# Kernel optimization log

Measured on AMD Instinct MI355X. Metric: run time of the kernel, lower is better.

Reference implementation:

```python
import jax, jax.numpy as jnp
import numpy as np

K = 32          # k_value
NUM_CLASSES = 10


def setup_inputs() -> dict:
    key = jax.random.key(0)
    k1, k2, k3 = jax.random.split(key, 3)
    queries = jax.random.normal(k1, (1024, 64), dtype=jnp.float32)
    train_data = jax.random.normal(k2, (200000, 64), dtype=jnp.float32)
    train_labels = jax.random.randint(k3, (200000,), 0, NUM_CLASSES, dtype=jnp.int32)
    return {"queries": queries, "train_data": train_data, "train_labels": train_labels}


def _votes(queries, train_data, train_labels):
    # Squared Euclidean distance [Q, N] via the ||q||^2 + ||x||^2 - 2 q.x expansion
    # (same math as sum of squared differences, O(Q*N*d) without a Q*N*d temp).
    q2 = jnp.sum(queries * queries, axis=1, keepdims=True)        # [Q, 1]
    x2 = jnp.sum(train_data * train_data, axis=1)                  # [N]
    sim = q2 + x2[None, :] - 2.0 * (queries @ train_data.T)        # [Q, N]
    sim = jnp.maximum(sim, 0.0)  # exact squared distances are >= 0
    # Inversion kernel: replace exact zeros with 0.1, then weights = 1/sim.
    sim = jnp.where(sim == 0.0, jnp.float32(0.1), sim)
    weights = 1.0 / sim                                            # [Q, N]
    # Top-K weights (largest weight == nearest neighbor).
    top_w, top_i = jax.lax.top_k(weights, K)                       # [Q, K]
    top_lab = train_labels[top_i]                                  # [Q, K] int
    # segment_sum over labels == scatter-add weights per class.
    Q = queries.shape[0]
    rows = jnp.arange(Q)[:, None]                                  # [Q, 1]
    votes = jnp.zeros((Q, NUM_CLASSES), dtype=top_w.dtype).at[rows, top_lab].add(top_w)
    return votes


def reference(queries, train_data, train_labels):
    votes = _votes(queries, train_data, train_labels)
    # argmax over class weight sums == tf.argmax(segment_sum) per query
    return jnp.argmax(votes, axis=1)
```

## Files before the change

kernel.cpp:

```cpp
#include <hip/hip_runtime.h>
#include <hip/hip_bf16.h>
#include <hip/hip_fp16.h>

#define N_TRAIN 200000
#define DIMS    64
#define NQ      1024
#define KSEL    32
#define NCLS    10

#define CHR     192
#define NCH     1048
#define LCAP    4
#define SENT    0xFFFFFFFFu
#define OVFCAP  256
#define TOTC    4096
#define MAXS    1536
#define SAMPLES 8192
#define SROWS   32
#define NPB     3125

typedef float f32x4 __attribute__((ext_vector_type(4)));
typedef short f16x8 __attribute__((ext_vector_type(8)));

__device__ __forceinline__ unsigned fmap(float f) {
    unsigned u = __float_as_uint(f);
    return u ^ ((u >> 31) ? 0xFFFFFFFFu : 0x80000000u);
}
__device__ __forceinline__ float funmap(unsigned m) {
    unsigned u = m ^ ((m >> 31) ? 0x80000000u : 0xFFFFFFFFu);
    return __uint_as_float(u);
}
__device__ __forceinline__ unsigned short f2h(float f) {
    union { __half h; unsigned short u; } c;
    c.h = __float2half_rn(f);
    return c.u;
}
__device__ __forceinline__ f16x8 pack8h(float4 a, float4 b) {
    f16x8 r;
    r[0] = (short)f2h(a.x); r[1] = (short)f2h(a.y);
    r[2] = (short)f2h(a.z); r[3] = (short)f2h(a.w);
    r[4] = (short)f2h(b.x); r[5] = (short)f2h(b.y);
    r[6] = (short)f2h(b.z); r[7] = (short)f2h(b.w);
    return r;
}

__global__ __launch_bounds__(512) void k_prep(const float* __restrict__ X,
                                              float* __restrict__ x2,
                                              float* __restrict__ bmax,
                                              short* __restrict__ Xh) {
    int T = blockIdx.x * 512 + threadIdx.x;
    int row = T >> 3;
    int l8 = T & 7;
    const float4* xp = (const float4*)(X + (long)row * 64 + l8 * 8);
    float4 a = xp[0], b = xp[1];
    *(f16x8*)(Xh + (long)row * 64 + l8 * 8) = pack8h(a, b);
    float p = a.x * a.x + a.y * a.y + a.z * a.z + a.w * a.w +
              b.x * b.x + b.y * b.y + b.z * b.z + b.w * b.w;
    p += __shfl_xor(p, 1);
    p += __shfl_xor(p, 2);
    p += __shfl_xor(p, 4);
    if (l8 == 0) x2[row] = p;
    float m = p;
    m = fmaxf(m, __shfl_xor(m, 8));
    m = fmaxf(m, __shfl_xor(m, 16));
    m = fmaxf(m, __shfl_xor(m, 32));
    __shared__ float wm[8];
    if ((threadIdx.x & 63) == 0) wm[threadIdx.x >> 6] = m;
    __syncthreads();
    if (threadIdx.x == 0) {
        float r = wm[0];
#pragma unroll
        for (int i = 1; i < 8; i++) r = fmaxf(r, wm[i]);
        bmax[blockIdx.x] = r;
    }
}

__global__ __launch_bounds__(256) void k_max(const float* __restrict__ bmax,
                                             float* __restrict__ x2maxf) {
    float m = -1e30f;
    for (int i = threadIdx.x; i < NPB; i += 256) m = fmaxf(m, bmax[i]);
#pragma unroll
    for (int d = 1; d < 64; d <<= 1) m = fmaxf(m, __shfl_xor(m, d));
    __shared__ float wm[4];
    if ((threadIdx.x & 63) == 0) wm[threadIdx.x >> 6] = m;
    __syncthreads();
    if (threadIdx.x == 0)
        *x2maxf = fmaxf(fmaxf(wm[0], wm[1]), fmaxf(wm[2], wm[3]));
}

__global__ __launch_bounds__(256) void k_cvt(const float* __restrict__ src,
                                             short* __restrict__ dst) {
    long c = (long)blockIdx.x * 256 + threadIdx.x;
    const float4* xp = (const float4*)(src + c * 8);
    float4 a = xp[0], b = xp[1];
    *(f16x8*)(dst + c * 8) = pack8h(a, b);
}

template<int MODE>
__global__ __launch_bounds__(64) void k_dist(
    const short* __restrict__ Xh, const short* __restrict__ Qh,
    const float* __restrict__ x2, const float* __restrict__ tqw,
    unsigned* __restrict__ pool,
    unsigned* __restrict__ ovfcnt, uint2* __restrict__ ovf,
    unsigned short* __restrict__ keys) {
    int bid = blockIdx.x;
    int qt, cb;
    if (MODE == 1) {
        qt = bid & 7;
        cb = bid >> 3;
    } else {
        int xcd = bid & 7;
        int j = bid >> 3;
        cb = xcd * 131 + (j >> 3);
        qt = j & 7;
    }
    int lane = threadIdx.x;
    int lr = lane & 15;
    int lk = lane >> 4;

    __shared__ unsigned lcnt[MODE == 0 ? 128 : 1];
    __shared__ unsigned lbuf[MODE == 0 ? 128 * LCAP : 1];

    int r0 = MODE ? cb * SROWS : cb * CHR;
    int rowEnd = MODE ? (r0 + SROWS) : min(r0 + CHR, N_TRAIN);

    if (MODE == 0) {
        lcnt[lane] = 0u;
        lcnt[lane + 64] = 0u;
        __syncthreads();
    }

    int qbase = qt << 7;

    f16x8 afr[8][2];
#pragma unroll
    for (int qi = 0; qi < 8; qi++) {
        const short* qp = Qh + (long)(qbase + (qi << 4) + lr) * 64 + (lk << 3);
        afr[qi][0] = *(const f16x8*)qp;
        afr[qi][1] = *(const f16x8*)(qp + 32);
    }
    float htq[8];
    if (MODE == 0) {
#pragma unroll
        for (int qi = 0; qi < 8; qi++) {
            float4 t4 = *(const float4*)(tqw + qbase + (qi << 4) + (lk << 2));
            htq[qi] = 0.5f * fmaxf(fmaxf(t4.x, t4.y), fmaxf(t4.z, t4.w));
        }
    }

    f16x8 cb0, cb1;
    float cx2;
    {
        int rowc = min(r0 + lr, rowEnd - 1);
        const short* xp = Xh + (long)rowc * 64 + (lk << 3);
        cb0 = *(const f16x8*)xp;
        cb1 = *(const f16x8*)(xp + 32);
        cx2 = (r0 + lr < rowEnd) ? x2[rowc] : 1e30f;
    }

    for (int base = r0; base < rowEnd; base += 16) {
        f16x8 b0 = cb0, b1 = cb1;
        float x2c = cx2;
        int nb = base + 16;
        if (nb < rowEnd) {
            int rowc = min(nb + lr, rowEnd - 1);
            const short* xp = Xh + (long)rowc * 64 + (lk << 3);
            cb0 = *(const f16x8*)xp;
            cb1 = *(const f16x8*)(xp + 32);
            cx2 = (nb + lr < rowEnd) ? x2[rowc] : 1e30f;
        }
        int row = base + lr;
        bool valid = row < rowEnd;
        float hx = 0.5f * x2c;

#pragma unroll
        for (int qi = 0; qi < 8; qi++) {
            f32x4 acc = {0.f, 0.f, 0.f, 0.f};
            acc = __builtin_amdgcn_mfma_f32_16x16x32_f16(afr[qi][0], b0, acc, 0, 0, 0);
            acc = __builtin_amdgcn_mfma_f32_16x16x32_f16(afr[qi][1], b1, acc, 0, 0, 0);
            if (MODE == 1) {
#pragma unroll
                for (int r4 = 0; r4 < 4; r4++) {
                    unsigned k16 = fmap(x2c - 2.f * acc[r4]) >> 16;
                    unsigned o = (unsigned)__shfl_xor((int)k16, 1);
                    unsigned v2 = k16 | (o << 16);
                    unsigned p2 = (unsigned)__shfl_xor((int)v2, 2);
                    if ((lr & 3) == 0) {
                        int qg = qbase + (qi << 4) + (lk << 2) + r4;
                        *(uint2*)(&keys[(long)qg * SAMPLES + row]) = make_uint2(v2, p2);
                    }
                }
            } else {
                float mx = fmaxf(fmaxf(acc[0], acc[1]), fmaxf(acc[2], acc[3]));
                if (valid && mx >= hx - htq[qi]) {
                    float4 t4 = *(const float4*)(tqw + qbase + (qi << 4) + (lk << 2));
                    float tq4[4] = {t4.x, t4.y, t4.z, t4.w};
#pragma unroll
                    for (int r4 = 0; r4 < 4; r4++) {
                        if (acc[r4] >= hx - 0.5f * tq4[r4]) {
                            int ql = (qi << 4) + (lk << 2) + r4;
                            int qg = qbase + ql;
                            unsigned entry = (fmap(x2c - 2.f * acc[r4]) & 0xFFFFFF00u) |
                                             (unsigned)(row - r0);
                            unsigned slot = atomicAdd(&lcnt[ql], 1u);
                            if (slot < LCAP) {
                                lbuf[ql * LCAP + slot] = entry;
                            } else {
                                unsigned o = atomicAdd(&ovfcnt[qg], 1u);
                                if (o < OVFCAP)
                                    ovf[qg * OVFCAP + o] =
                                        make_uint2(entry >> 8, (unsigned)row);
                            }
                        }
                    }
                }
            }
        }
    }

    if (MODE == 0) {
        __syncthreads();
#pragma unroll
        for (int j = 0; j < 2; j++) {
            int ql = (j << 6) + lane;
            unsigned lc = min(lcnt[ql], (unsigned)LCAP);
            uint4 v;
            v.x = (lc > 0) ? lbuf[ql * LCAP + 0] : SENT;
            v.y = (lc > 1) ? lbuf[ql * LCAP + 1] : SENT;
            v.z = (lc > 2) ? lbuf[ql * LCAP + 2] : SENT;
            v.w = (lc > 3) ? lbuf[ql * LCAP + 3] : SENT;
            *(uint4*)&pool[((long)cb * NQ + qbase + ql) * LCAP] = v;
        }
    }
}

__global__ __launch_bounds__(256) void k_sel(const unsigned short* __restrict__ keys,
                                             const float* __restrict__ Qm,
                                             const float* __restrict__ x2maxf,
                                             float* __restrict__ tqw,
                                             float* __restrict__ q2g) {
    int q = blockIdx.x, tid = threadIdx.x;
    unsigned short mk[32];
#pragma unroll
    for (int m = 0; m < 32; m++) mk[m] = keys[(long)q * SAMPLES + tid + 256 * m];
    __shared__ float q2s_;
    __shared__ int cnt;
    if (tid < 64) {
        float v = Qm[(long)q * 64 + tid];
        float p = v * v;
#pragma unroll
        for (int d = 1; d < 64; d <<= 1) p += __shfl_xor(p, d);
        if (tid == 0) q2s_ = p;
    }
    unsigned lo = 0, hi = 65535;
    for (int it = 0; it < 16; ++it) {
        __syncthreads();
        if (tid == 0) cnt = 0;
        __syncthreads();
        unsigned mid = (lo + hi) >> 1;
        int c = 0;
#pragma unroll
        for (int m = 0; m < 32; m++) c += (mk[m] <= mid) ? 1 : 0;
#pragma unroll
        for (int d = 1; d < 64; d <<= 1) c += __shfl_xor(c, d);
        if ((tid & 63) == 0) atomicAdd(&cnt, c);
        __syncthreads();
        if (cnt >= KSEL) hi = mid; else lo = mid + 1;
    }
    if (tid == 0) {
        unsigned vv = hi + 2u; if (vv > 65535u) vv = 65535u;
        float t = funmap(vv << 16);
        float q2 = q2s_;
        tqw[q] = t + 0.004f * sqrtf(q2 * (*x2maxf)) + 0.1f;
        q2g[q] = q2;
    }
}

__global__ __launch_bounds__(256) void k_merge(const float* __restrict__ Qm,
                                               const float* __restrict__ X,
                                               const float* __restrict__ x2,
                                               const int* __restrict__ labels,
                                               const unsigned* __restrict__ pool,
                                               const unsigned* __restrict__ ovfcnt,
                                               const uint2* __restrict__ ovf,
                                               const float* __restrict__ q2g,
                                               const float* __restrict__ x2maxf,
                                               int* __restrict__ out) {
    int q = blockIdx.x, tid = threadIdx.x;
    __shared__ unsigned eK[TOTC];
    __shared__ int eR[TOTC];
    __shared__ int sR[MAXS];
    __shared__ float sKey[MAXS];
    __shared__ int sLab[MAXS];
    __shared__ float qs[64];
    __shared__ int tot, cnt, ns, nw, nt;
    __shared__ unsigned cutS;
    __shared__ float wKey[34];
    __shared__ int wLab[34];
    __shared__ int tIdx[64];
    __shared__ int tLab[64];

    if (tid == 0) { tot = 0; ns = 0; nw = 0; nt = 0; }
    if (tid < 64) qs[tid] = Qm[(long)q * 64 + tid];
    __syncthreads();

    for (int c2 = tid; c2 < NCH; c2 += 256) {
        uint4 v = *(const uint4*)&pool[((long)c2 * NQ + q) * LCAP];
        int rbase = c2 * CHR;
        if (v.x != SENT) { int p = atomicAdd(&tot, 1); if (p < TOTC) { eK[p] = v.x >> 8; eR[p] = rbase + (int)(v.x & 255u); } }
        if (v.y != SENT) { int p = atomicAdd(&tot, 1); if (p < TOTC) { eK[p] = v.y >> 8; eR[p] = rbase + (int)(v.y & 255u); } }
        if (v.z != SENT) { int p = atomicAdd(&tot, 1); if (p < TOTC) { eK[p] = v.z >> 8; eR[p] = rbase + (int)(v.z & 255u); } }
        if (v.w != SENT) { int p = atomicAdd(&tot, 1); if (p < TOTC) { eK[p] = v.w >> 8; eR[p] = rbase + (int)(v.w & 255u); } }
    }
    int ov = min((int)ovfcnt[q], OVFCAP);
    for (int i = tid; i < ov; i += 256) {
        uint2 e = ovf[q * OVFCAP + i];
        int p = atomicAdd(&tot, 1);
        if (p < TOTC) { eK[p] = e.x; eR[p] = (int)e.y; }
    }
    __syncthreads();
    int T = min(tot, TOTC);

    unsigned mk[16];
#pragma unroll
    for (int m = 0; m < 16; m++) { int i = tid + (m << 8); mk[m] = (i < T) ? eK[i] : 0xFFFFFFFFu; }
    unsigned lo = 0, hi = 0xFFFFFFu;
    for (int it = 0; it < 24; ++it) {
        __syncthreads();
        if (tid == 0) cnt = 0;
        __syncthreads();
        unsigned mid = (lo + hi) >> 1;
        int c = 0;
#pragma unroll
        for (int m = 0; m < 16; m++) c += (mk[m] <= mid) ? 1 : 0;
#pragma unroll
        for (int d = 1; d < 64; d <<= 1) c += __shfl_xor(c, d);
        if ((tid & 63) == 0) atomicAdd(&cnt, c);
        __syncthreads();
        if (cnt >= KSEL) hi = mid; else lo = mid + 1;
    }
    float q2v = q2g[q];
    if (tid == 0) {
        unsigned vv = min(hi + 1u, 0xFFFFFFu);
        float tf = funmap(vv << 8);
        float err = 0.004f * sqrtf(q2v * (*x2maxf)) + 0.1f;
        cutS = min((fmap(tf + err) >> 8) + 1u, 0xFFFFFFu);
    }
    __syncthreads();
    unsigned cut = cutS;
    for (int i = tid; i < T; i += 256)
        if (eK[i] <= cut) { int p = atomicAdd(&ns, 1); if (p < MAXS) sR[p] = eR[i]; }
    __syncthreads();
    int NS = min(ns, MAXS);

    for (int i = tid; i < NS; i += 256) {
        int row = sR[i];
        const float4* xr = (const float4*)(X + (long)row * 64);
        const float4* qr = (const float4*)qs;
        float dot = 0.f;
#pragma unroll
        for (int k4 = 0; k4 < 16; k4++) {
            float4 xv = xr[k4], qv = qr[k4];
            dot += qv.x * xv.x + qv.y * xv.y + qv.z * xv.z + qv.w * xv.w;
        }
        sKey[i] = x2[row] - 2.f * dot;
        sLab[i] = labels[row];
    }
    __syncthreads();

    unsigned uk[6];
#pragma unroll
    for (int m = 0; m < 6; m++) { int i = tid + (m << 8); uk[m] = (i < NS) ? fmap(sKey[i]) : 0xFFFFFFFFu; }
    unsigned lo2 = 0u, hi2 = 0xFFFFFFFFu;
    for (int it = 0; it < 32; ++it) {
        __syncthreads();
        if (tid == 0) cnt = 0;
        __syncthreads();
        unsigned mid = lo2 + ((hi2 - lo2) >> 1);
        int c = 0;
#pragma unroll
        for (int m = 0; m < 6; m++) c += (uk[m] <= mid) ? 1 : 0;
#pragma unroll
        for (int d = 1; d < 64; d <<= 1) c += __shfl_xor(c, d);
        if ((tid & 63) == 0) atomicAdd(&cnt, c);
        __syncthreads();
        if (cnt >= KSEL) hi2 = mid; else lo2 = mid + 1;
    }
    unsigned T32 = hi2;

#pragma unroll
    for (int m = 0; m < 6; m++) {
        int i = tid + (m << 8);
        if (i < NS) {
            if (uk[m] < T32) {
                int p = atomicAdd(&nw, 1);
                if (p < 34) { wKey[p] = sKey[i]; wLab[p] = sLab[i]; }
            } else if (uk[m] == T32) {
                int p = atomicAdd(&nt, 1);
                if (p < 64) { tIdx[p] = sR[i]; tLab[p] = sLab[i]; }
            }
        }
    }
    __syncthreads();

    if (tid == 0) {
        float votes[NCLS] = {0.f, 0.f, 0.f, 0.f, 0.f, 0.f, 0.f, 0.f, 0.f, 0.f};
        int NW = min(nw, 32);
        for (int i = 0; i < NW; i++) {
            float dist = q2v + wKey[i];
            if (dist < 0.f) dist = 0.f;
            if (dist == 0.f) dist = 0.1f;
            votes[wLab[i]] += 1.f / dist;
        }
        int need = KSEL - NW;
        int NT = min(nt, 64);
        float tkey = funmap(T32);
        float dist = q2v + tkey;
        if (dist < 0.f) dist = 0.f;
        if (dist == 0.f) dist = 0.1f;
        float twgt = 1.f / dist;
        for (int t = 0; t < need && t < NT; t++) {
            int best = -1, bi = 0x7FFFFFFF;
            for (int u = 0; u < NT; u++)
                if (tIdx[u] < bi) { bi = tIdx[u]; best = u; }
            if (best < 0) break;
            votes[tLab[best]] += twgt;
            tIdx[best] = 0x7FFFFFFF;
        }
        float bv = votes[0];
        int bc = 0;
#pragma unroll
        for (int c = 1; c < NCLS; c++)
            if (votes[c] > bv) { bv = votes[c]; bc = c; }
        out[q] = bc;
    }
}

extern "C" void kernel_launch(void* const* d_in, const int* in_sizes, int n_in,
                              void* d_out, int out_size, void* d_ws, size_t ws_size,
                              hipStream_t stream) {
    const float* Qm = (const float*)d_in[0];
    const float* X = (const float*)d_in[1];
    const int* labels = (const int*)d_in[2];
    char* ws = (char*)d_ws;
    float* x2 = (float*)(ws + 0);
    float* tqw = (float*)(ws + 800000);
    float* q2g = (float*)(ws + 804096);
    float* x2maxf = (float*)(ws + 808192);
    float* bmax = (float*)(ws + 808256);
    unsigned* ovfcnt = (unsigned*)(ws + 820800);
    uint2* ovf = (uint2*)(ws + 824896);
    unsigned* pool = (unsigned*)(ws + 2922048);
    unsigned short* keys = (unsigned short*)(ws + 2922048);
    short* Xh = (short*)(ws + 20092480);
    short* Qh = (short*)(ws + 45692480);
    int* out = (int*)d_out;

    hipMemsetAsync(ovfcnt, 0, 4096, stream);
    k_prep<<<NPB, 512, 0, stream>>>(X, x2, bmax, Xh);
    k_max<<<1, 256, 0, stream>>>(bmax, x2maxf);
    k_cvt<<<32, 256, 0, stream>>>(Qm, Qh);
    k_dist<1><<<8 * (SAMPLES / SROWS), 64, 0, stream>>>(Xh, Qh, x2, tqw, pool, ovfcnt, ovf, keys);
    k_sel<<<NQ, 256, 0, stream>>>(keys, Qm, x2maxf, tqw, q2g);
    k_dist<0><<<8 * NCH, 64, 0, stream>>>(Xh, Qh, x2, tqw, pool, ovfcnt, ovf, keys);
    k_merge<<<NQ, 256, 0, stream>>>(Qm, X, x2, labels, pool, ovfcnt, ovf, q2g, x2maxf, out);
}
```

Measured before the change: 269.5 us.

## Fuse sample distance computation into threshold selection kernel using fp32 dots

Removes the separate MFMA sampling pass that wrote 16-bit keys to global memory. The selection kernel now computes fp32 dot products of each query against 4096 sample rows directly into shared memory, then bisects the full 32-bit key space. This cuts one launch and the global key round-trip and halves the sample count. In exchange each query block reads the sample rows itself with scalar fp32 math, which may be slower than the MFMA path, and the smaller sample may loosen the threshold.

```diff
diff --git a/kernel.cpp b/kernel.cpp
--- a/kernel.cpp
+++ b/kernel.cpp
@@ -15,8 +15,7 @@
 #define OVFCAP  256
 #define TOTC    4096
 #define MAXS    1536
-#define SAMPLES 8192
-#define SROWS   32
+#define SAMPLES 4096
 #define NPB     3125
 
 typedef float f32x4 __attribute__((ext_vector_type(4)));
@@ -96,39 +95,97 @@
     *(f16x8*)(dst + c * 8) = pack8h(a, b);
 }
 
-template<int MODE>
+__global__ __launch_bounds__(256) void k_sel(const float* __restrict__ X,
+                                             const float* __restrict__ Qm,
+                                             const float* __restrict__ x2,
+                                             const float* __restrict__ x2maxf,
+                                             float* __restrict__ tqw,
+                                             float* __restrict__ q2g) {
+    int q = blockIdx.x, tid = threadIdx.x;
+    __shared__ float qs[64];
+    __shared__ unsigned skey[SAMPLES];
+    __shared__ float q2s_;
+    __shared__ int cnt;
+
+    if (tid < 64) qs[tid] = Qm[(long)q * 64 + tid];
+    __syncthreads();
+    if (tid < 64) {
+        float v = qs[tid];
+        float p = v * v;
+#pragma unroll
+        for (int d = 1; d < 64; d <<= 1) p += __shfl_xor(p, d);
+        if (tid == 0) q2s_ = p;
+    }
+
+    int l4 = tid & 3;
+    float4 qf[4];
+#pragma unroll
+    for (int k = 0; k < 4; k++) qf[k] = ((const float4*)qs)[l4 * 4 + k];
+
+    for (int it = 0; it < SAMPLES / 64; it++) {
+        int row = (it << 6) + (tid >> 2);
+        const float4* xr = (const float4*)(X + (long)row * 64 + l4 * 16);
+        float dot = 0.f;
+#pragma unroll
+        for (int k = 0; k < 4; k++) {
+            float4 xv = xr[k];
+            dot += qf[k].x * xv.x + qf[k].y * xv.y + qf[k].z * xv.z + qf[k].w * xv.w;
+        }
+        dot += __shfl_xor(dot, 1);
+        dot += __shfl_xor(dot, 2);
+        if (l4 == 0) skey[row] = fmap(x2[row] - 2.f * dot);
+    }
+    __syncthreads();
+
+    unsigned mk[SAMPLES / 256];
+#pragma unroll
+    for (int m = 0; m < SAMPLES / 256; m++) mk[m] = skey[tid + 256 * m];
+    unsigned lo = 0u, hi = 0xFFFFFFFFu;
+    for (int itb = 0; itb < 32; ++itb) {
+        __syncthreads();
+        if (tid == 0) cnt = 0;
+        __syncthreads();
+        unsigned mid = lo + ((hi - lo) >> 1);
+        int c = 0;
+#pragma unroll
+        for (int m = 0; m < SAMPLES / 256; m++) c += (mk[m] <= mid) ? 1 : 0;
+#pragma unroll
+        for (int d = 1; d < 64; d <<= 1) c += __shfl_xor(c, d);
+        if ((tid & 63) == 0) atomicAdd(&cnt, c);
+        __syncthreads();
+        if (cnt >= KSEL) hi = mid; else lo = mid + 1;
+    }
+    if (tid == 0) {
+        float t = funmap(hi);
+        float q2 = q2s_;
+        tqw[q] = t + 0.004f * sqrtf(q2 * (*x2maxf)) + 0.1f;
+        q2g[q] = q2;
+    }
+}
+
 __global__ __launch_bounds__(64) void k_dist(
     const short* __restrict__ Xh, const short* __restrict__ Qh,
     const float* __restrict__ x2, const float* __restrict__ tqw,
     unsigned* __restrict__ pool,
-    unsigned* __restrict__ ovfcnt, uint2* __restrict__ ovf,
-    unsigned short* __restrict__ keys) {
+    unsigned* __restrict__ ovfcnt, uint2* __restrict__ ovf) {
     int bid = blockIdx.x;
-    int qt, cb;
-    if (MODE == 1) {
-        qt = bid & 7;
-        cb = bid >> 3;
-    } else {
-        int xcd = bid & 7;
-        int j = bid >> 3;
-        cb = xcd * 131 + (j >> 3);
-        qt = j & 7;
-    }
+    int xcd = bid & 7;
+    int j = bid >> 3;
+    int cb = xcd * 131 + (j >> 3);
+    int qt = j & 7;
     int lane = threadIdx.x;
     int lr = lane & 15;
     int lk = lane >> 4;
 
-    __shared__ unsigned lcnt[MODE == 0 ? 128 : 1];
-    __shared__ unsigned lbuf[MODE == 0 ? 128 * LCAP : 1];
-
-    int r0 = MODE ? cb * SROWS : cb * CHR;
-    int rowEnd = MODE ? (r0 + SROWS) : min(r0 + CHR, N_TRAIN);
-
-    if (MODE == 0) {
-        lcnt[lane] = 0u;
-        lcnt[lane + 64] = 0u;
-        __syncthreads();
-    }
+    __shared__ unsigned lcnt[128];
+    __shared__ unsigned lbuf[128 * LCAP];
+
+    int r0 = cb * CHR;
+    int rowEnd = min(r0 + CHR, N_TRAIN);
+
+    lcnt[lane] = 0u;
+    lcnt[lane + 64] = 0u;
+    __syncthreads();
 
     int qbase = qt << 7;
 
@@ -140,12 +197,10 @@
         afr[qi][1] = *(const f16x8*)(qp + 32);
     }
     float htq[8];
-    if (MODE == 0) {
-#pragma unroll
-        for (int qi = 0; qi < 8; qi++) {
-            float4 t4 = *(const float4*)(tqw + qbase + (qi << 4) + (lk << 2));
-            htq[qi] = 0.5f * fmaxf(fmaxf(t4.x, t4.y), fmaxf(t4.z, t4.w));
-        }
+#pragma unroll
+    for (int qi = 0; qi < 8; qi++) {
+        float4 t4 = *(const float4*)(tqw + qbase + (qi << 4) + (lk << 2));
+        htq[qi] = 0.5f * fmaxf(fmaxf(t4.x, t4.y), fmaxf(t4.z, t4.w));
     }
 
     f16x8 cb0, cb1;
@@ -178,39 +233,25 @@
             f32x4 acc = {0.f, 0.f, 0.f, 0.f};
             acc = __builtin_amdgcn_mfma_f32_16x16x32_f16(afr[qi][0], b0, acc, 0, 0, 0);
             acc = __builtin_amdgcn_mfma_f32_16x16x32_f16(afr[qi][1], b1, acc, 0, 0, 0);
-            if (MODE == 1) {
+            float mx = fmaxf(fmaxf(acc[0], acc[1]), fmaxf(acc[2], acc[3]));
+            if (valid && mx >= hx - htq[qi]) {
+                float4 t4 = *(const float4*)(tqw + qbase + (qi << 4) + (lk << 2));
+                float tq4[4] = {t4.x, t4.y, t4.z, t4.w};
 #pragma unroll
                 for (int r4 = 0; r4 < 4; r4++) {
-                    unsigned k16 = fmap(x2c - 2.f * acc[r4]) >> 16;
-                    unsigned o = (unsigned)__shfl_xor((int)k16, 1);
-                    unsigned v2 = k16 | (o << 16);
-                    unsigned p2 = (unsigned)__shfl_xor((int)v2, 2);
-                    if ((lr & 3) == 0) {
-                        int qg = qbase + (qi << 4) + (lk << 2) + r4;
-                        *(uint2*)(&keys[(long)qg * SAMPLES + row]) = make_uint2(v2, p2);
-                    }
-                }
-            } else {
-                float mx = fmaxf(fmaxf(acc[0], acc[1]), fmaxf(acc[2], acc[3]));
-                if (valid && mx >= hx - htq[qi]) {
-                    float4 t4 = *(const float4*)(tqw + qbase + (qi << 4) + (lk << 2));
-                    float tq4[4] = {t4.x, t4.y, t4.z, t4.w};
-#pragma unroll
-                    for (int r4 = 0; r4 < 4; r4++) {
-                        if (acc[r4] >= hx - 0.5f * tq4[r4]) {
-                            int ql = (qi << 4) + (lk << 2) + r4;
-                            int qg = qbase + ql;
-                            unsigned entry = (fmap(x2c - 2.f * acc[r4]) & 0xFFFFFF00u) |
-                                             (unsigned)(row - r0);
-                            unsigned slot = atomicAdd(&lcnt[ql], 1u);
-                            if (slot < LCAP) {
-                                lbuf[ql * LCAP + slot] = entry;
-                            } else {
-                                unsigned o = atomicAdd(&ovfcnt[qg], 1u);
-                                if (o < OVFCAP)
-                                    ovf[qg * OVFCAP + o] =
-                                        make_uint2(entry >> 8, (unsigned)row);
-                            }
+                    if (acc[r4] >= hx - 0.5f * tq4[r4]) {
+                        int ql = (qi << 4) + (lk << 2) + r4;
+                        int qg = qbase + ql;
+                        unsigned entry = (fmap(x2c - 2.f * acc[r4]) & 0xFFFFFF00u) |
+                                         (unsigned)(row - r0);
+                        unsigned slot = atomicAdd(&lcnt[ql], 1u);
+                        if (slot < LCAP) {
+                            lbuf[ql * LCAP + slot] = entry;
+                        } else {
+                            unsigned o = atomicAdd(&ovfcnt[qg], 1u);
+                            if (o < OVFCAP)
+                                ovf[qg * OVFCAP + o] =
+                                    make_uint2(entry >> 8, (unsigned)row);
                         }
                     }
                 }
@@ -218,61 +259,17 @@
         }
     }
 
-    if (MODE == 0) {
-        __syncthreads();
-#pragma unroll
-        for (int j = 0; j < 2; j++) {
-            int ql = (j << 6) + lane;
-            unsigned lc = min(lcnt[ql], (unsigned)LCAP);
-            uint4 v;
-            v.x = (lc > 0) ? lbuf[ql * LCAP + 0] : SENT;
-            v.y = (lc > 1) ? lbuf[ql * LCAP + 1] : SENT;
-            v.z = (lc > 2) ? lbuf[ql * LCAP + 2] : SENT;
-            v.w = (lc > 3) ? lbuf[ql * LCAP + 3] : SENT;
-            *(uint4*)&pool[((long)cb * NQ + qbase + ql) * LCAP] = v;
-        }
-    }
-}
-
-__global__ __launch_bounds__(256) void k_sel(const unsigned short* __restrict__ keys,
-                                             const float* __restrict__ Qm,
-                                             const float* __restrict__ x2maxf,
-                                             float* __restrict__ tqw,
-                                             float* __restrict__ q2g) {
-    int q = blockIdx.x, tid = threadIdx.x;
-    unsigned short mk[32];
-#pragma unroll
-    for (int m = 0; m < 32; m++) mk[m] = keys[(long)q * SAMPLES + tid + 256 * m];
-    __shared__ float q2s_;
-    __shared__ int cnt;
-    if (tid < 64) {
-        float v = Qm[(long)q * 64 + tid];
-        float p = v * v;
-#pragma unroll
-        for (int d = 1; d < 64; d <<= 1) p += __shfl_xor(p, d);
-        if (tid == 0) q2s_ = p;
-    }
-    unsigned lo = 0, hi = 65535;
-    for (int it = 0; it < 16; ++it) {
-        __syncthreads();
-        if (tid == 0) cnt = 0;
-        __syncthreads();
-        unsigned mid = (lo + hi) >> 1;
-        int c = 0;
-#pragma unroll
-        for (int m = 0; m < 32; m++) c += (mk[m] <= mid) ? 1 : 0;
-#pragma unroll
-        for (int d = 1; d < 64; d <<= 1) c += __shfl_xor(c, d);
-        if ((tid & 63) == 0) atomicAdd(&cnt, c);
-        __syncthreads();
-        if (cnt >= KSEL) hi = mid; else lo = mid + 1;
-    }
-    if (tid == 0) {
-        unsigned vv = hi + 2u; if (vv > 65535u) vv = 65535u;
-        float t = funmap(vv << 16);
-        float q2 = q2s_;
-        tqw[q] = t + 0.004f * sqrtf(q2 * (*x2maxf)) + 0.1f;
-        q2g[q] = q2;
+    __syncthreads();
+#pragma unroll
+    for (int j2 = 0; j2 < 2; j2++) {
+        int ql = (j2 << 6) + lane;
+        unsigned lc = min(lcnt[ql], (unsigned)LCAP);
+        uint4 v;
+        v.x = (lc > 0) ? lbuf[ql * LCAP + 0] : SENT;
+        v.y = (lc > 1) ? lbuf[ql * LCAP + 1] : SENT;
+        v.z = (lc > 2) ? lbuf[ql * LCAP + 2] : SENT;
+        v.w = (lc > 3) ? lbuf[ql * LCAP + 3] : SENT;
+        *(uint4*)&pool[((long)cb * NQ + qbase + ql) * LCAP] = v;
     }
 }
 
@@ -451,7 +448,6 @@
     unsigned* ovfcnt = (unsigned*)(ws + 820800);
     uint2* ovf = (uint2*)(ws + 824896);
     unsigned* pool = (unsigned*)(ws + 2922048);
-    unsigned short* keys = (unsigned short*)(ws + 2922048);
     short* Xh = (short*)(ws + 20092480);
     short* Qh = (short*)(ws + 45692480);
     int* out = (int*)d_out;
@@ -460,8 +456,7 @@
     k_prep<<<NPB, 512, 0, stream>>>(X, x2, bmax, Xh);
     k_max<<<1, 256, 0, stream>>>(bmax, x2maxf);
     k_cvt<<<32, 256, 0, stream>>>(Qm, Qh);
-    k_dist<1><<<8 * (SAMPLES / SROWS), 64, 0, stream>>>(Xh, Qh, x2, tqw, pool, ovfcnt, ovf, keys);
-    k_sel<<<NQ, 256, 0, stream>>>(keys, Qm, x2maxf, tqw, q2g);
-    k_dist<0><<<8 * NCH, 64, 0, stream>>>(Xh, Qh, x2, tqw, pool, ovfcnt, ovf, keys);
+    k_sel<<<NQ, 256, 0, stream>>>(X, Qm, x2, x2maxf, tqw, q2g);
+    k_dist<<<8 * NCH, 64, 0, stream>>>(Xh, Qh, x2, tqw, pool, ovfcnt, ovf);
     k_merge<<<NQ, 256, 0, stream>>>(Qm, X, x2, labels, pool, ovfcnt, ovf, q2g, x2maxf, out);
 }
```

Measured after the change: 349.1 us. +29.5%, slower.
